# Optimization experiments

Hardware: AMD Instinct MI355X
Metric: run time of the kernel (lower is better)

## Reference

```python
import jax, jax.numpy as jnp
import numpy as np

INPUT_DIM, HIDDEN, LAYERS, PRED_LEN = 4, 80, 5, 48
BATCH, SEQ = 512, 336


def _lstm_stack_step(inp, h, c, Wih0, Wih, Whh, bih, bhh):
    # inp: (B, D_in); h, c: (L, B, H). PyTorch gate order: i, f, g, o.
    hs, cs = [], []
    for l in range(LAYERS):
        W = Wih0 if l == 0 else Wih[l - 1]
        gates = inp @ W.T + h[l] @ Whh[l].T + bih[l] + bhh[l]
        i, f, g, o = jnp.split(gates, 4, axis=-1)
        c_new = jax.nn.sigmoid(f) * c[l] + jax.nn.sigmoid(i) * jnp.tanh(g)
        h_new = jax.nn.sigmoid(o) * jnp.tanh(c_new)
        hs.append(h_new); cs.append(c_new)
        inp = h_new
    return jnp.stack(hs), jnp.stack(cs), inp


def setup_inputs() -> dict:
    key = jax.random.key(0)
    ks = jax.random.split(key, 16)
    s = 1.0 / np.sqrt(HIDDEN)
    u = lambda k, shape: jax.random.uniform(k, shape, jnp.float32, -s, s)
    G = 4 * HIDDEN
    return {
        "x": jax.random.normal(ks[0], (BATCH, SEQ, INPUT_DIM), jnp.float32),
        "future_features": jax.random.normal(ks[1], (BATCH, PRED_LEN, INPUT_DIM - 1), jnp.float32),
        "enc_Wih0": u(ks[2], (G, INPUT_DIM)),
        "enc_Wih": u(ks[3], (LAYERS - 1, G, HIDDEN)),
        "enc_Whh": u(ks[4], (LAYERS, G, HIDDEN)),
        "enc_bih": u(ks[5], (LAYERS, G)),
        "enc_bhh": u(ks[6], (LAYERS, G)),
        "dec_Wih0": u(ks[7], (G, INPUT_DIM)),
        "dec_Wih": u(ks[8], (LAYERS - 1, G, HIDDEN)),
        "dec_Whh": u(ks[9], (LAYERS, G, HIDDEN)),
        "dec_bih": u(ks[10], (LAYERS, G)),
        "dec_bhh": u(ks[11], (LAYERS, G)),
        "fc_W": u(ks[12], (1, HIDDEN)),
        "fc_b": u(ks[13], (1,)),
    }


def reference(x, future_features, enc_Wih0, enc_Wih, enc_Whh, enc_bih, enc_bhh,
              dec_Wih0, dec_Wih, dec_Whh, dec_bih, dec_bhh, fc_W, fc_b):
    B = x.shape[0]
    h0 = jnp.zeros((LAYERS, B, HIDDEN), x.dtype)
    c0 = jnp.zeros((LAYERS, B, HIDDEN), x.dtype)

    # ---- Encoder: scan over time, keep only final (h, c) ----
    def enc_step(carry, x_t):
        h, c = carry
        h, c, _ = _lstm_stack_step(x_t, h, c, enc_Wih0, enc_Wih, enc_Whh, enc_bih, enc_bhh)
        return (h, c), None

    (h, c), _ = jax.lax.scan(enc_step, (h0, c0), jnp.swapaxes(x, 0, 1))

    def dec_step(carry, ff_t):
        h, c, inp = carry
        h, c, top = _lstm_stack_step(inp, h, c, dec_Wih0, dec_Wih, dec_Whh, dec_bih, dec_bhh)
        pred = top @ fc_W.T + fc_b            # (B, 1)
        next_inp = jnp.concatenate([pred, ff_t], axis=-1)  # (B, INPUT_DIM)
        return (h, c, next_inp), pred[:, 0]

    init_inp = x[:, -1, :]
    _, preds = jax.lax.scan(dec_step, (h, c, init_inp), jnp.swapaxes(future_features, 0, 1))
    return jnp.swapaxes(preds, 0, 1)  # (B, pred_len)
```

## Files before the change

kernel.cpp:

```cpp
#include <hip/hip_runtime.h>
#include <hip/hip_fp16.h>
#include <math.h>

#define LAYERS  5
#define HID     80
#define GATES   320
#define INDIM   4
#define BATCH   512
#define SEQLEN  336
#define PREDLEN 48
#define TOT     (SEQLEN + PREDLEN)
#define NB      4
#define ENB     2
#define NTHR    800
#define NSUP    (SEQLEN + LAYERS - 1)

#define BSTR 96
#define LSTR (ENB * BSTR)
#define HTOT (LAYERS * LSTR)
#define CSZ  (LAYERS * ENB * HID)
#define M16B 48
#define M16L (ENB * M16B)
#define MSZ  (LAYERS * M16L)

#define NE16    32000
#define ND4     64000
#define OFF_D   NE16
#define OFF_BE  (NE16 + ND4)
#define OFF_BD  (OFF_BE + 400)
#define OFF_W0D (OFF_BD + 400)
#define NWS4    (OFF_W0D + 1280)
#define WS_NEED ((size_t)NWS4 * 16)
#define NPREP   NWS4

__device__ __forceinline__ float sigm(float v) { return 1.0f / (1.0f + __expf(-v)); }
__device__ __forceinline__ float tanh_fast(float v) {
    return 1.0f - 2.0f / (1.0f + __expf(2.0f * v));
}
__device__ __forceinline__ float gate_act(float v, bool tg) {
    const float e = __expf(tg ? 2.0f * v : -v);
    const float r = 1.0f / (1.0f + e);
    return tg ? 1.0f - 2.0f * r : r;
}
__device__ __forceinline__ float rs4(float v0, float v1, float v2, float v3, int q) {
    float u = (q & 1) ? v1 : v0;
    float s = (q & 1) ? v0 : v1;
    u += __shfl_xor(s, 1);
    float u2 = (q & 1) ? v3 : v2;
    float s2 = (q & 1) ? v2 : v3;
    u2 += __shfl_xor(s2, 1);
    float k = (q & 2) ? u2 : u;
    float s3 = (q & 2) ? u : u2;
    k += __shfl_xor(s3, 2);
    return k;
}

__device__ __forceinline__ unsigned h2bits(__half2 h) {
    union { __half2 h; unsigned u; } c; c.h = h; return c.u;
}

typedef _Float16 h2v __attribute__((ext_vector_type(2)));
__device__ __forceinline__ float dot2f(unsigned wu, unsigned hu, float acc) {
    union { unsigned u; h2v v; } cw, ch;
    cw.u = wu; ch.u = hu;
#if __has_builtin(__builtin_amdgcn_fdot2)
    return __builtin_amdgcn_fdot2(cw.v, ch.v, acc, false);
#else
    acc = fmaf((float)cw.v[0], (float)ch.v[0], acc);
    return fmaf((float)cw.v[1], (float)ch.v[1], acc);
#endif
}

#define DOT16(U0, U1, H)                                                         \
    do {                                                                         \
        a[0][0] = dot2f((U0).x, (H)[0].x, a[0][0]);                              \
        a[0][0] = dot2f((U0).y, (H)[0].y, a[0][0]);                              \
        a[0][1] = dot2f((U0).x, (H)[1].x, a[0][1]);                              \
        a[0][1] = dot2f((U0).y, (H)[1].y, a[0][1]);                              \
        a[1][0] = dot2f((U0).z, (H)[0].x, a[1][0]);                              \
        a[1][0] = dot2f((U0).w, (H)[0].y, a[1][0]);                              \
        a[1][1] = dot2f((U0).z, (H)[1].x, a[1][1]);                              \
        a[1][1] = dot2f((U0).w, (H)[1].y, a[1][1]);                              \
        a[2][0] = dot2f((U1).x, (H)[0].x, a[2][0]);                              \
        a[2][0] = dot2f((U1).y, (H)[0].y, a[2][0]);                              \
        a[2][1] = dot2f((U1).x, (H)[1].x, a[2][1]);                              \
        a[2][1] = dot2f((U1).y, (H)[1].y, a[2][1]);                              \
        a[3][0] = dot2f((U1).z, (H)[0].x, a[3][0]);                              \
        a[3][0] = dot2f((U1).w, (H)[0].y, a[3][0]);                              \
        a[3][1] = dot2f((U1).z, (H)[1].x, a[3][1]);                              \
        a[3][1] = dot2f((U1).w, (H)[1].y, a[3][1]);                              \
    } while (0)

#define FMA8(W, H)                                                               \
    do {                                                                         \
        _Pragma("unroll")                                                        \
        for (int _j = 0; _j < 4; ++_j) {                                         \
            _Pragma("unroll")                                                    \
            for (int _b = 0; _b < 2; ++_b)                                       \
                a[_j][_b] += (W)[_j].x * (H)[_b].x + (W)[_j].y * (H)[_b].y       \
                           + (W)[_j].z * (H)[_b].z + (W)[_j].w * (H)[_b].w;      \
        }                                                                        \
    } while (0)

#define LDH16(SET, C)                                                            \
    do {                                                                         \
        (SET)[0] = *(const uint2*)(mb + 2 * (C));                                \
        (SET)[1] = *(const uint2*)(mb + M16B + 2 * (C));                         \
    } while (0)

__global__ void prep_pack(const float* __restrict__ eW0,  const float* __restrict__ eWih,
                          const float* __restrict__ eWhh, const float* __restrict__ ebih,
                          const float* __restrict__ ebhh,
                          const float* __restrict__ dW0,  const float* __restrict__ dWih,
                          const float* __restrict__ dWhh, const float* __restrict__ dbih,
                          const float* __restrict__ dbhh, float* __restrict__ ws)
{
    const int gid = blockIdx.x * 256 + threadIdx.x;
    float4* w4 = (float4*)ws;
    if (gid < NE16) {
        const int lt = gid % 160;
        const int p  = (gid / 160) & 1;
        const int i  = (gid / 320) % 20;
        const int wl = gid / 6400;
        const int m = lt >> 1, mat = lt & 1;
        float4 f[2];
        #pragma unroll
        for (int g = 0; g < 2; ++g) {
            const int j = 2 * p + g;
            const int row = m + 80 * j;
            float4 v = make_float4(0.f, 0.f, 0.f, 0.f);
            if (wl > 0) {
                v = mat ? *(const float4*)&eWih[((size_t)(wl - 1) * GATES + row) * HID + 4 * i]
                        : *(const float4*)&eWhh[((size_t)wl * GATES + row) * HID + 4 * i];
            } else if (!mat) {
                if (i < 10) v = *(const float4*)&eWhh[(size_t)row * HID + 4 * i];
            } else {
                if (i < 10)       v = *(const float4*)&eWhh[(size_t)row * HID + 40 + 4 * i];
                else if (i == 10) v = *(const float4*)&eW0[row * INDIM];
            }
            f[g] = v;
        }
        uint4 u;
        u.x = h2bits(__floats2half2_rn(f[0].x, f[0].y));
        u.y = h2bits(__floats2half2_rn(f[0].z, f[0].w));
        u.z = h2bits(__floats2half2_rn(f[1].x, f[1].y));
        u.w = h2bits(__floats2half2_rn(f[1].z, f[1].w));
        ((uint4*)ws)[gid] = u;
        return;
    }
    int g2 = gid - NE16;
    if (g2 < ND4) {
        const int lt = g2 % 320;
        const int j  = (g2 / 320) & 3;
        const int i  = (g2 / 1280) % 10;
        const int l  = g2 / 12800;
        const int dm = lt >> 2, dmat = (lt >> 1) & 1, dkh = lt & 1;
        const int row = dm + 80 * j;
        const int k0  = dkh * 40 + 4 * i;
        float4 v = make_float4(0.f, 0.f, 0.f, 0.f);
        if (l == 0) {
            if (!dmat) v = *(const float4*)&dWhh[(size_t)row * HID + k0];
        } else {
            v = dmat ? *(const float4*)&dWih[((size_t)(l - 1) * GATES + row) * HID + k0]
                     : *(const float4*)&dWhh[((size_t)l * GATES + row) * HID + k0];
        }
        w4[OFF_D + g2] = v;
        return;
    }
    int g3 = g2 - ND4;
    if (g3 < 800) {
        const int ctx = g3 / 400, r = g3 % 400;
        const int l = r / 80, m = r % 80;
        const float* bi = ctx ? dbih : ebih;
        const float* bh = ctx ? dbhh : ebhh;
        float4 v;
        v.x = bi[l * GATES + m]       + bh[l * GATES + m];
        v.y = bi[l * GATES + m + 80]  + bh[l * GATES + m + 80];
        v.z = bi[l * GATES + m + 160] + bh[l * GATES + m + 160];
        v.w = bi[l * GATES + m + 240] + bh[l * GATES + m + 240];
        w4[OFF_BE + g3] = v;
        return;
    }
    int g4 = g3 - 800;
    if (g4 < 1280) {
        const int lt = g4 % 320, j = g4 / 320;
        const int dm = lt >> 2;
        w4[OFF_W0D + g4] = *(const float4*)&dW0[(dm + 80 * j) * INDIM];
    }
}

__global__ __launch_bounds__(NTHR, 1) void lstm_main(
    const float* __restrict__ x,   const float* __restrict__ ff,
    const float* __restrict__ fcW, const float* __restrict__ fcb,
    const float* __restrict__ ws,  float* __restrict__ out)
{
    __shared__ __align__(16) float hA[HTOT];
    __shared__ __align__(16) float hB[HTOT];
    __shared__ __align__(16) unsigned mA16[MSZ];
    __shared__ __align__(16) unsigned mB16[MSZ];
    __shared__ __align__(16) float cS[CSZ];
    __shared__ __align__(16) float sx[ENB][4];

    const uint4*  w16 = (const uint4*)ws;
    const float4* w4d = (const float4*)ws + OFF_D;
    const float4* b4e = (const float4*)ws + OFF_BE;
    const float4* b4d = (const float4*)ws + OFF_BD;
    const float4* w0d = (const float4*)ws + OFF_W0D;

    const int tid = threadIdx.x;
    const int b0  = blockIdx.x * ENB;

    for (int i = tid; i < HTOT; i += NTHR) { hA[i] = 0.0f; hB[i] = 0.0f; }
    for (int i = tid; i < MSZ;  i += NTHR) { mA16[i] = 0u; mB16[i] = 0u; }
    for (int i = tid; i < CSZ;  i += NTHR) cS[i] = 0.0f;
    if (tid < ENB) {
        const float4 xv = *(const float4*)&x[((size_t)(b0 + tid) * SEQLEN) * INDIM];
        __half* mx = (__half*)mB16 + (size_t)tid * 96 + 80;
        mx[0] = __float2half(xv.x); mx[1] = __float2half(xv.y);
        mx[2] = __float2half(xv.z); mx[3] = __float2half(xv.w);
    }
    __syncthreads();

    const int wl    = tid / 160;
    const int lt    = tid % 160;
    const int em    = lt >> 1;
    const int emat  = lt & 1;
    const int nquad = (wl == 0) ? 3 : 5;

    #pragma unroll 1
    for (int s = 0; s < NSUP; ++s) {
        float*    cur  = (s & 1) ? hB : hA;
        unsigned* mcur = (s & 1) ? mB16 : mA16;
        unsigned* mprv = (s & 1) ? mA16 : mB16;
        const int t = s - wl;

        if (tid < ENB && s + 1 < SEQLEN) {
            const float4 xv = *(const float4*)&x[((size_t)(b0 + tid) * SEQLEN + (s + 1)) * INDIM];
            __half* mx = (__half*)mcur + (size_t)tid * 96 + 80;
            mx[0] = __float2half(xv.x); mx[1] = __float2half(xv.y);
            mx[2] = __float2half(xv.z); mx[3] = __float2half(xv.w);
        }

        if (t >= 0 && t < SEQLEN) {
            const unsigned* mb = emat ? (wl ? mprv + (wl - 1) * M16L : mprv + 20)
                                      : mprv + wl * M16L;
            const uint4* wq = w16 + (size_t)wl * 6400 + lt;

            uint4 u0a = wq[0],   u0b = wq[160];
            uint4 u1a = wq[320], u1b = wq[480];
            uint4 u2a = wq[640], u2b = wq[800];
            uint4 u3a = wq[960], u3b = wq[1120];
            uint2 h0[2], h1[2], h2[2], h3[2];
            LDH16(h0, 0); LDH16(h1, 1); LDH16(h2, 2); LDH16(h3, 3);

            float a[4][2];
            #pragma unroll
            for (int j = 0; j < 4; ++j) { a[j][0] = 0.0f; a[j][1] = 0.0f; }

            #pragma unroll 1
            for (int q4 = 0; q4 < nquad - 1; ++q4) {
                const int c = 4 * q4;
                DOT16(u0a, u0b, h0); u0a = wq[1280]; u0b = wq[1440]; LDH16(h0, c + 4);
                DOT16(u1a, u1b, h1); u1a = wq[1600]; u1b = wq[1760]; LDH16(h1, c + 5);
                DOT16(u2a, u2b, h2); u2a = wq[1920]; u2b = wq[2080]; LDH16(h2, c + 6);
                DOT16(u3a, u3b, h3); u3a = wq[2240]; u3b = wq[2400]; LDH16(h3, c + 7);
                wq += 1280;
            }
            DOT16(u0a, u0b, h0);
            DOT16(u1a, u1b, h1);
            DOT16(u2a, u2b, h2);
            DOT16(u3a, u3b, h3);

            float sA[4];
            #pragma unroll
            for (int j = 0; j < 4; ++j)
                sA[j] = a[j][emat] + __shfl_xor(a[j][emat ^ 1], 1);

            const float4 bv = b4e[wl * 80 + em];
            const float gi = sigm(sA[0] + bv.x);
            const float gf = sigm(sA[1] + bv.y);
            const float gg = tanh_fast(sA[2] + bv.z);
            const float go = sigm(sA[3] + bv.w);
            const int ci = wl * (ENB * HID) + emat * HID + em;
            const float cn = gf * cS[ci] + gi * gg;
            cS[ci] = cn;
            const float hn = go * tanh_fast(cn);
            cur[wl * LSTR + emat * BSTR + em] = hn;
            ((__half*)mcur)[(size_t)(wl * 2 + emat) * 96 + em] = __float2half(hn);
        }
        __syncthreads();
    }

    for (int i = tid; i < 2 * LSTR; i += NTHR) {
        const int l = (i < LSTR) ? 1 : 3;
        const int off = i % LSTR;
        hB[l * LSTR + off] = hA[l * LSTR + off];
    }
    if (tid < ENB * INDIM)
        sx[tid >> 2][tid & 3] =
            x[((size_t)(b0 + (tid >> 2)) * SEQLEN + (SEQLEN - 1)) * INDIM + (tid & 3)];
    __syncthreads();

    const int dm   = tid >> 2;
    const int dmat = (tid >> 1) & 1;
    const int dkh  = tid & 1;

    #pragma unroll 1
    for (int t = SEQLEN; t < TOT; ++t) {
        float* cur = (t & 1) ? hB : hA;
        float* prv = (t & 1) ? hA : hB;

        #pragma unroll 1
        for (int l = 0; l < LAYERS; ++l) {
            if (tid < 320) {
                float a[4][2];
                #pragma unroll
                for (int j = 0; j < 4; ++j) { a[j][0] = 0.0f; a[j][1] = 0.0f; }

                if (l == 0 && dmat) {
                    if (dkh == 0) {
                        const float4 xv0 = *(const float4*)&sx[0][0];
                        const float4 xv1 = *(const float4*)&sx[1][0];
                        #pragma unroll
                        for (int j = 0; j < 4; ++j) {
                            const float4 w0v = w0d[j * 320 + tid];
                            a[j][0] += w0v.x * xv0.x + w0v.y * xv0.y + w0v.z * xv0.z + w0v.w * xv0.w;
                            a[j][1] += w0v.x * xv1.x + w0v.y * xv1.y + w0v.z * xv1.z + w0v.w * xv1.w;
                        }
                    }
                } else {
                    const float* hb = (dmat ? cur + (l - 1) * LSTR : prv + l * LSTR)
                                      + dkh * 40;
                    const float4* wp = w4d + (size_t)l * 12800 + tid;
                    float4 wv[4];
                    wv[0] = wp[0]; wv[1] = wp[320]; wv[2] = wp[640]; wv[3] = wp[960];

                    #pragma unroll 1
                    for (int i = 0; i < 9; ++i) {
                        const float4* np = wp + 1280;
                        float4 nv[4];
                        nv[0] = np[0]; nv[1] = np[320]; nv[2] = np[640]; nv[3] = np[960];
                        float4 hv[2];
                        hv[0] = *(const float4*)(hb + 4 * i);
                        hv[1] = *(const float4*)(hb + BSTR + 4 * i);
                        FMA8(wv, hv);
                        #pragma unroll
                        for (int j = 0; j < 4; ++j) wv[j] = nv[j];
                        wp = np;
                    }
                    {
                        float4 hv[2];
                        hv[0] = *(const float4*)(hb + 36);
                        hv[1] = *(const float4*)(hb + BSTR + 36);
                        FMA8(wv, hv);
                    }
                }

                float s[4];
                #pragma unroll
                for (int j = 0; j < 4; ++j)
                    s[j] = a[j][dkh] + __shfl_xor(a[j][dkh ^ 1], 1);
                #pragma unroll
                for (int j = 0; j < 4; ++j)
                    s[j] += __shfl_xor(s[j], 2);

                const float4 bv = b4d[l * 80 + dm];
                float act0, act1;
                if (!dmat) { act0 = sigm(s[0] + bv.x);      act1 = sigm(s[1] + bv.y); }
                else       { act0 = tanh_fast(s[2] + bv.z); act1 = sigm(s[3] + bv.w); }
                const float o0 = __shfl_xor(act0, 2);
                const float o1 = __shfl_xor(act1, 2);
                if (!dmat) {
                    const float gi = act0, gf = act1, gg = o0, go = o1;
                    const int ci = l * (ENB * HID) + dkh * HID + dm;
                    const float cn = gf * cS[ci] + gi * gg;
                    cS[ci] = cn;
                    cur[l * LSTR + dkh * BSTR + dm] = go * tanh_fast(cn);
                }
            }
            __syncthreads();
        }

        const int td = t - SEQLEN;
        if (tid < ENB) {
            float s = fcb[0];
            const float* hvp = cur + 4 * LSTR + tid * BSTR;
            #pragma unroll
            for (int jj = 0; jj < HID; jj += 4) {
                const float4 wv4 = *(const float4*)&fcW[jj];
                const float4 h4  = *(const float4*)&hvp[jj];
                s += wv4.x * h4.x + wv4.y * h4.y + wv4.z * h4.z + wv4.w * h4.w;
            }
            out[(size_t)(b0 + tid) * PREDLEN + td] = s;
            sx[tid][0] = s;
        } else if (tid >= 64 && tid < 64 + ENB * 3) {
            const int qd = tid - 64;
            const int nb = qd / 3, k = qd % 3;
            sx[nb][k + 1] = ff[((size_t)(b0 + nb) * PREDLEN + td) * 3 + k];
        }
        __syncthreads();
    }
}

#define FQK 20
#define FCHUNK(WPTR, HPTR, I)                                                    \
    do {                                                                         \
        const float4 wA = *(const float4*)((WPTR) + 4 * (I));                    \
        const float4 wB = *(const float4*)((WPTR) + HID + 4 * (I));              \
        const float* _hb = (HPTR);                                               \
        const float4 h0 = *(const float4*)(_hb + 0 * HID + 4 * (I));             \
        const float4 h1 = *(const float4*)(_hb + 1 * HID + 4 * (I));             \
        const float4 h2 = *(const float4*)(_hb + 2 * HID + 4 * (I));             \
        const float4 h3 = *(const float4*)(_hb + 3 * HID + 4 * (I));             \
        a00 += wA.x * h0.x + wA.y * h0.y + wA.z * h0.z + wA.w * h0.w;            \
        a01 += wA.x * h1.x + wA.y * h1.y + wA.z * h1.z + wA.w * h1.w;            \
        a02 += wA.x * h2.x + wA.y * h2.y + wA.z * h2.z + wA.w * h2.w;            \
        a03 += wA.x * h3.x + wA.y * h3.y + wA.z * h3.z + wA.w * h3.w;            \
        a10 += wB.x * h0.x + wB.y * h0.y + wB.z * h0.z + wB.w * h0.w;            \
        a11 += wB.x * h1.x + wB.y * h1.y + wB.z * h1.z + wB.w * h1.w;            \
        a12 += wB.x * h2.x + wB.y * h2.y + wB.z * h2.z + wB.w * h2.w;            \
        a13 += wB.x * h3.x + wB.y * h3.y + wB.z * h3.z + wB.w * h3.w;            \
    } while (0)

__global__ __launch_bounds__(640) void lstm_fb(
    const float* __restrict__ x,    const float* __restrict__ ff,
    const float* __restrict__ eW0,  const float* __restrict__ eWih,
    const float* __restrict__ eWhh, const float* __restrict__ ebih,
    const float* __restrict__ ebhh,
    const float* __restrict__ dW0,  const float* __restrict__ dWih,
    const float* __restrict__ dWhh, const float* __restrict__ dbih,
    const float* __restrict__ dbhh,
    const float* __restrict__ fcW,  const float* __restrict__ fcb,
    float* __restrict__ out)
{
    __shared__ __align__(16) float sh[LAYERS][NB][HID];
    __shared__ __align__(16) float sc[LAYERS][NB][HID];
    __shared__ __align__(16) float sg[NB][GATES + 1];
    __shared__ __align__(16) float sx[NB][INDIM];

    const int tid = threadIdx.x;
    const int q   = tid & 3;
    const int mm  = tid >> 2;
    const int r0  = 2 * mm;
    const int b0  = blockIdx.x * NB;

    for (int i = tid; i < LAYERS * NB * HID; i += 640) {
        (&sh[0][0][0])[i] = 0.0f;
        (&sc[0][0][0])[i] = 0.0f;
    }
    const bool is_tg = (r0 >= 2 * HID) && (r0 < 3 * HID);
    const int  unb = tid / HID, uj = tid % HID;

    float bs[2][LAYERS][2];
    #pragma unroll
    for (int l = 0; l < LAYERS; ++l) {
        bs[0][l][0] = ebih[l * GATES + r0]     + ebhh[l * GATES + r0];
        bs[0][l][1] = ebih[l * GATES + r0 + 1] + ebhh[l * GATES + r0 + 1];
        bs[1][l][0] = dbih[l * GATES + r0]     + dbhh[l * GATES + r0];
        bs[1][l][1] = dbih[l * GATES + r0 + 1] + dbhh[l * GATES + r0 + 1];
    }
    const float w0e0 = eW0[r0 * INDIM + q], w0e1 = eW0[(r0 + 1) * INDIM + q];
    const float w0d0 = dW0[r0 * INDIM + q], w0d1 = dW0[(r0 + 1) * INDIM + q];

    for (int t = 0; t < TOT; ++t) {
        const bool enc = (t < SEQLEN);
        const float* Wih = enc ? eWih : dWih;
        const float* Whh = enc ? eWhh : dWhh;
        if (enc && tid < NB * INDIM) {
            const int nb = tid / INDIM, k = tid % INDIM;
            sx[nb][k] = x[((size_t)(b0 + nb) * SEQLEN + t) * INDIM + k];
        }
        __syncthreads();
        #pragma unroll
        for (int l = 0; l < LAYERS; ++l) {
            float a00 = 0.f, a01 = 0.f, a02 = 0.f, a03 = 0.f;
            float a10 = 0.f, a11 = 0.f, a12 = 0.f, a13 = 0.f;
            {
                const float* wp = Whh + ((size_t)l * GATES + r0) * HID + q * FQK;
                const float* hp = &sh[l][0][q * FQK];
                #pragma unroll
                for (int i = 0; i < FQK / 4; ++i) FCHUNK(wp, hp, i);
            }
            if (l == 0) {
                const float wa = enc ? w0e0 : w0d0;
                const float wb = enc ? w0e1 : w0d1;
                a00 += wa * sx[0][q];  a01 += wa * sx[1][q];
                a02 += wa * sx[2][q];  a03 += wa * sx[3][q];
                a10 += wb * sx[0][q];  a11 += wb * sx[1][q];
                a12 += wb * sx[2][q];  a13 += wb * sx[3][q];
            } else {
                const float* wp = Wih + ((size_t)(l - 1) * GATES + r0) * HID + q * FQK;
                const float* hp = &sh[l - 1][0][q * FQK];
                #pragma unroll
                for (int i = 0; i < FQK / 4; ++i) FCHUNK(wp, hp, i);
            }
            const float s0 = rs4(a00, a01, a02, a03, q);
            const float s1 = rs4(a10, a11, a12, a13, q);
            const float bias0 = enc ? bs[0][l][0] : bs[1][l][0];
            const float bias1 = enc ? bs[0][l][1] : bs[1][l][1];
            sg[q][r0]     = gate_act(s0 + bias0, is_tg);
            sg[q][r0 + 1] = gate_act(s1 + bias1, is_tg);
            __syncthreads();
            if (tid < NB * HID) {
                const float iv = sg[unb][uj];
                const float fv = sg[unb][uj + HID];
                const float gv = sg[unb][uj + 2 * HID];
                const float ov = sg[unb][uj + 3 * HID];
                const float cn = fv * sc[l][unb][uj] + iv * gv;
                const float hn = ov * tanh_fast(cn);
                sc[l][unb][uj] = cn;
                sh[l][unb][uj] = hn;
            }
            __syncthreads();
        }
        if (!enc) {
            const int td = t - SEQLEN;
            if (tid < NB) {
                float s = fcb[0];
                #pragma unroll
                for (int j = 0; j < HID; j += 4) {
                    const float4 wv = *(const float4*)&fcW[j];
                    const float4 hv = *(const float4*)&sh[LAYERS - 1][tid][j];
                    s += wv.x * hv.x + wv.y * hv.y + wv.z * hv.z + wv.w * hv.w;
                }
                out[(size_t)(b0 + tid) * PREDLEN + td] = s;
                sx[tid][0] = s;
            } else if (tid >= 64 && tid < 64 + NB * 3) {
                const int qd = tid - 64;
                const int nb = qd / 3, k = qd % 3;
                sx[nb][k + 1] = ff[((size_t)(b0 + nb) * PREDLEN + td) * 3 + k];
            }
        }
    }
}

extern "C" void kernel_launch(void* const* d_in, const int* in_sizes, int n_in,
                              void* d_out, int out_size, void* d_ws, size_t ws_size,
                              hipStream_t stream) {
    const float* x    = (const float*)d_in[0];
    const float* ff   = (const float*)d_in[1];
    const float* eW0  = (const float*)d_in[2];
    const float* eWih = (const float*)d_in[3];
    const float* eWhh = (const float*)d_in[4];
    const float* ebih = (const float*)d_in[5];
    const float* ebhh = (const float*)d_in[6];
    const float* dW0  = (const float*)d_in[7];
    const float* dWih = (const float*)d_in[8];
    const float* dWhh = (const float*)d_in[9];
    const float* dbih = (const float*)d_in[10];
    const float* dbhh = (const float*)d_in[11];
    const float* fcW  = (const float*)d_in[12];
    const float* fcb  = (const float*)d_in[13];

    if (ws_size >= WS_NEED) {
        prep_pack<<<(NPREP + 255) / 256, 256, 0, stream>>>(
            eW0, eWih, eWhh, ebih, ebhh, dW0, dWih, dWhh, dbih, dbhh, (float*)d_ws);
        lstm_main<<<BATCH / ENB, NTHR, 0, stream>>>(
            x, ff, fcW, fcb, (const float*)d_ws, (float*)d_out);
    } else {
        lstm_fb<<<BATCH / NB, 640, 0, stream>>>(
            x, ff, eW0, eWih, eWhh, ebih, ebhh,
            dW0, dWih, dWhh, dbih, dbhh, fcW, fcb, (float*)d_out);
    }
}
```

Baseline: 2.649 ms.

## Store decoder weights as fp16 and cache encoder layer-1 weights in LDS

Decoder weights are now packed as fp16 pairs instead of fp32 float4, which halves the bytes read per step; they are converted back to fp32 and used in FMAs against fp32 hidden states. The encoder layer-1 weight slice (about 100KB) is also copied into shared memory once per block, so that wavefront reads from LDS instead of global memory. The trade-offs are reduced decoder weight precision, extra conversion instructions, and a large LDS footprint that may limit occupancy or exceed per-block limits.

Measured after the change: 2.508 ms. -5.3%, faster.

```diff
diff --git a/kernel.cpp b/kernel.cpp
--- a/kernel.cpp
+++ b/kernel.cpp
@@ -24,9 +24,9 @@
 #define MSZ  (LAYERS * M16L)
 
 #define NE16    32000
-#define ND4     64000
+#define ND16    32000
 #define OFF_D   NE16
-#define OFF_BE  (NE16 + ND4)
+#define OFF_BE  (NE16 + ND16)
 #define OFF_BD  (OFF_BE + 400)
 #define OFF_W0D (OFF_BD + 400)
 #define NWS4    (OFF_W0D + 1280)
@@ -70,6 +70,27 @@
     return fmaf((float)cw.v[1], (float)ch.v[1], acc);
 #endif
 }
+
+__device__ __forceinline__ void fma_mix4(float& acc, unsigned w01, unsigned w23,
+                                         const float4& h) {
+    union { unsigned u; __half2 h2; } c01, c23;
+    c01.u = w01; c23.u = w23;
+    acc = fmaf(__half2float(__low2half(c01.h2)),  h.x, acc);
+    acc = fmaf(__half2float(__high2half(c01.h2)), h.y, acc);
+    acc = fmaf(__half2float(__low2half(c23.h2)),  h.z, acc);
+    acc = fmaf(__half2float(__high2half(c23.h2)), h.w, acc);
+}
+#define MIXCHUNK(U0, U1, H)                                                      \
+    do {                                                                         \
+        fma_mix4(a[0][0], (U0).x, (U0).y, (H)[0]);                               \
+        fma_mix4(a[0][1], (U0).x, (U0).y, (H)[1]);                               \
+        fma_mix4(a[1][0], (U0).z, (U0).w, (H)[0]);                               \
+        fma_mix4(a[1][1], (U0).z, (U0).w, (H)[1]);                               \
+        fma_mix4(a[2][0], (U1).x, (U1).y, (H)[0]);                               \
+        fma_mix4(a[2][1], (U1).x, (U1).y, (H)[1]);                               \
+        fma_mix4(a[3][0], (U1).z, (U1).w, (H)[0]);                               \
+        fma_mix4(a[3][1], (U1).z, (U1).w, (H)[1]);                               \
+    } while (0)
 
 #define DOT16(U0, U1, H)                                                         \
     do {                                                                         \
@@ -91,21 +112,34 @@
         a[3][1] = dot2f((U1).w, (H)[1].y, a[3][1]);                              \
     } while (0)
 
-#define FMA8(W, H)                                                               \
-    do {                                                                         \
-        _Pragma("unroll")                                                        \
-        for (int _j = 0; _j < 4; ++_j) {                                         \
-            _Pragma("unroll")                                                    \
-            for (int _b = 0; _b < 2; ++_b)                                       \
-                a[_j][_b] += (W)[_j].x * (H)[_b].x + (W)[_j].y * (H)[_b].y       \
-                           + (W)[_j].z * (H)[_b].z + (W)[_j].w * (H)[_b].w;      \
-        }                                                                        \
-    } while (0)
-
 #define LDH16(SET, C)                                                            \
     do {                                                                         \
         (SET)[0] = *(const uint2*)(mb + 2 * (C));                                \
         (SET)[1] = *(const uint2*)(mb + M16B + 2 * (C));                         \
+    } while (0)
+
+#define ENC_DOT(WQ)                                                              \
+    do {                                                                         \
+        const uint4* wq = (WQ);                                                  \
+        uint4 u0a = wq[0],   u0b = wq[160];                                      \
+        uint4 u1a = wq[320], u1b = wq[480];                                      \
+        uint4 u2a = wq[640], u2b = wq[800];                                      \
+        uint4 u3a = wq[960], u3b = wq[1120];                                     \
+        uint2 h0[2], h1[2], h2[2], h3[2];                                        \
+        LDH16(h0, 0); LDH16(h1, 1); LDH16(h2, 2); LDH16(h3, 3);                  \
+        _Pragma("unroll 1")                                                      \
+        for (int q4 = 0; q4 < nquad - 1; ++q4) {                                 \
+            const int c = 4 * q4;                                                \
+            DOT16(u0a, u0b, h0); u0a = wq[1280]; u0b = wq[1440]; LDH16(h0, c + 4);\
+            DOT16(u1a, u1b, h1); u1a = wq[1600]; u1b = wq[1760]; LDH16(h1, c + 5);\
+            DOT16(u2a, u2b, h2); u2a = wq[1920]; u2b = wq[2080]; LDH16(h2, c + 6);\
+            DOT16(u3a, u3b, h3); u3a = wq[2240]; u3b = wq[2400]; LDH16(h3, c + 7);\
+            wq += 1280;                                                          \
+        }                                                                        \
+        DOT16(u0a, u0b, h0);                                                     \
+        DOT16(u1a, u1b, h1);                                                     \
+        DOT16(u2a, u2b, h2);                                                     \
+        DOT16(u3a, u3b, h3);                                                     \
     } while (0)
 
 __global__ void prep_pack(const float* __restrict__ eW0,  const float* __restrict__ eWih,
@@ -149,25 +183,36 @@
         return;
     }
     int g2 = gid - NE16;
-    if (g2 < ND4) {
+    if (g2 < ND16) {
         const int lt = g2 % 320;
-        const int j  = (g2 / 320) & 3;
-        const int i  = (g2 / 1280) % 10;
-        const int l  = g2 / 12800;
+        const int p  = (g2 / 320) & 1;
+        const int i  = (g2 / 640) % 10;
+        const int l  = g2 / 6400;
         const int dm = lt >> 2, dmat = (lt >> 1) & 1, dkh = lt & 1;
-        const int row = dm + 80 * j;
-        const int k0  = dkh * 40 + 4 * i;
-        float4 v = make_float4(0.f, 0.f, 0.f, 0.f);
-        if (l == 0) {
-            if (!dmat) v = *(const float4*)&dWhh[(size_t)row * HID + k0];
-        } else {
-            v = dmat ? *(const float4*)&dWih[((size_t)(l - 1) * GATES + row) * HID + k0]
-                     : *(const float4*)&dWhh[((size_t)l * GATES + row) * HID + k0];
-        }
-        w4[OFF_D + g2] = v;
+        const int k0 = dkh * 40 + 4 * i;
+        float4 f[2];
+        #pragma unroll
+        for (int g = 0; g < 2; ++g) {
+            const int j = 2 * p + g;
+            const int row = dm + 80 * j;
+            float4 v = make_float4(0.f, 0.f, 0.f, 0.f);
+            if (l == 0) {
+                if (!dmat) v = *(const float4*)&dWhh[(size_t)row * HID + k0];
+            } else {
+                v = dmat ? *(const float4*)&dWih[((size_t)(l - 1) * GATES + row) * HID + k0]
+                         : *(const float4*)&dWhh[((size_t)l * GATES + row) * HID + k0];
+            }
+            f[g] = v;
+        }
+        uint4 u;
+        u.x = h2bits(__floats2half2_rn(f[0].x, f[0].y));
+        u.y = h2bits(__floats2half2_rn(f[0].z, f[0].w));
+        u.z = h2bits(__floats2half2_rn(f[1].x, f[1].y));
+        u.w = h2bits(__floats2half2_rn(f[1].z, f[1].w));
+        ((uint4*)ws)[OFF_D + g2] = u;
         return;
     }
-    int g3 = g2 - ND4;
+    int g3 = g2 - ND16;
     if (g3 < 800) {
         const int ctx = g3 / 400, r = g3 % 400;
         const int l = r / 80, m = r % 80;
@@ -194,6 +239,7 @@
     const float* __restrict__ fcW, const float* __restrict__ fcb,
     const float* __restrict__ ws,  float* __restrict__ out)
 {
+    __shared__ __align__(16) uint4 wlds[6400];
     __shared__ __align__(16) float hA[HTOT];
     __shared__ __align__(16) float hB[HTOT];
     __shared__ __align__(16) unsigned mA16[MSZ];
@@ -201,15 +247,16 @@
     __shared__ __align__(16) float cS[CSZ];
     __shared__ __align__(16) float sx[ENB][4];
 
-    const uint4*  w16 = (const uint4*)ws;
-    const float4* w4d = (const float4*)ws + OFF_D;
-    const float4* b4e = (const float4*)ws + OFF_BE;
-    const float4* b4d = (const float4*)ws + OFF_BD;
-    const float4* w0d = (const float4*)ws + OFF_W0D;
+    const uint4*  w16  = (const uint4*)ws;
+    const uint4*  w16d = w16 + OFF_D;
+    const float4* b4e  = (const float4*)ws + OFF_BE;
+    const float4* b4d  = (const float4*)ws + OFF_BD;
+    const float4* w0d  = (const float4*)ws + OFF_W0D;
 
     const int tid = threadIdx.x;
     const int b0  = blockIdx.x * ENB;
 
+    for (int i = tid; i < 6400; i += NTHR) wlds[i] = w16[6400 + i];
     for (int i = tid; i < HTOT; i += NTHR) { hA[i] = 0.0f; hB[i] = 0.0f; }
     for (int i = tid; i < MSZ;  i += NTHR) { mA16[i] = 0u; mB16[i] = 0u; }
     for (int i = tid; i < CSZ;  i += NTHR) cS[i] = 0.0f;
@@ -244,32 +291,15 @@
         if (t >= 0 && t < SEQLEN) {
             const unsigned* mb = emat ? (wl ? mprv + (wl - 1) * M16L : mprv + 20)
                                       : mprv + wl * M16L;
-            const uint4* wq = w16 + (size_t)wl * 6400 + lt;
-
-            uint4 u0a = wq[0],   u0b = wq[160];
-            uint4 u1a = wq[320], u1b = wq[480];
-            uint4 u2a = wq[640], u2b = wq[800];
-            uint4 u3a = wq[960], u3b = wq[1120];
-            uint2 h0[2], h1[2], h2[2], h3[2];
-            LDH16(h0, 0); LDH16(h1, 1); LDH16(h2, 2); LDH16(h3, 3);
-
             float a[4][2];
             #pragma unroll
             for (int j = 0; j < 4; ++j) { a[j][0] = 0.0f; a[j][1] = 0.0f; }
 
-            #pragma unroll 1
-            for (int q4 = 0; q4 < nquad - 1; ++q4) {
-                const int c = 4 * q4;
-                DOT16(u0a, u0b, h0); u0a = wq[1280]; u0b = wq[1440]; LDH16(h0, c + 4);
-                DOT16(u1a, u1b, h1); u1a = wq[1600]; u1b = wq[1760]; LDH16(h1, c + 5);
-                DOT16(u2a, u2b, h2); u2a = wq[1920]; u2b = wq[2080]; LDH16(h2, c + 6);
-                DOT16(u3a, u3b, h3); u3a = wq[2240]; u3b = wq[2400]; LDH16(h3, c + 7);
-                wq += 1280;
-            }
-            DOT16(u0a, u0b, h0);
-            DOT16(u1a, u1b, h1);
-            DOT16(u2a, u2b, h2);
-            DOT16(u3a, u3b, h3);
+            if (wl == 1) {
+                ENC_DOT(wlds + lt);
+            } else {
+                ENC_DOT(w16 + (size_t)wl * 6400 + lt);
+            }
 
             float sA[4];
             #pragma unroll
@@ -331,28 +361,23 @@
                 } else {
                     const float* hb = (dmat ? cur + (l - 1) * LSTR : prv + l * LSTR)
                                       + dkh * 40;
-                    const float4* wp = w4d + (size_t)l * 12800 + tid;
-                    float4 wv[4];
-                    wv[0] = wp[0]; wv[1] = wp[320]; wv[2] = wp[640]; wv[3] = wp[960];
+                    const uint4* wp = w16d + (size_t)l * 6400 + tid;
+                    uint4 u0 = wp[0], u1 = wp[320];
 
                     #pragma unroll 1
                     for (int i = 0; i < 9; ++i) {
-                        const float4* np = wp + 1280;
-                        float4 nv[4];
-                        nv[0] = np[0]; nv[1] = np[320]; nv[2] = np[640]; nv[3] = np[960];
+                        const uint4 n0 = wp[640], n1 = wp[960];
                         float4 hv[2];
                         hv[0] = *(const float4*)(hb + 4 * i);
                         hv[1] = *(const float4*)(hb + BSTR + 4 * i);
-                        FMA8(wv, hv);
-                        #pragma unroll
-                        for (int j = 0; j < 4; ++j) wv[j] = nv[j];
-                        wp = np;
+                        MIXCHUNK(u0, u1, hv);
+                        u0 = n0; u1 = n1; wp += 640;
                     }
                     {
                         float4 hv[2];
                         hv[0] = *(const float4*)(hb + 36);
                         hv[1] = *(const float4*)(hb + BSTR + 36);
-                        FMA8(wv, hv);
+                        MIXCHUNK(u0, u1, hv);
                     }
                 }
 
```
